# Kernel optimization log

Measured on AMD Instinct MI355X. Metric: run time of the kernel, lower is better.

Reference implementation:

```python
import jax, jax.numpy as jnp
import numpy as np

D_MODEL = 1024
D_STATE = 16
D_CONV = 4
EXPAND = 2
D_INNER = EXPAND * D_MODEL          # 2048
DT_RANK = D_INNER // 16             # 128
BATCH = 2
SEQLEN = 1024


def _silu(x):
    return x * jax.nn.sigmoid(x)


def setup_inputs() -> dict:
    key = jax.random.key(0)
    ks = jax.random.split(key, 8)
    s = 0.02
    A_init = jnp.tile(jnp.arange(1, D_STATE + 1, dtype=jnp.float32)[None, :], (D_INNER, 1))
    return {
        "x": jax.random.normal(ks[0], (BATCH, SEQLEN, D_MODEL), jnp.float32),
        "W_in": jax.random.normal(ks[1], (D_MODEL, 2 * D_INNER), jnp.float32) * s,
        "conv_k": jax.random.normal(ks[2], (D_CONV, 1, D_INNER), jnp.float32) * s,  # (kw, in/groups, out)
        "conv_b": jnp.zeros((D_INNER,), jnp.float32),
        "W_xproj": jax.random.normal(ks[3], (D_INNER, DT_RANK + 2 * D_STATE), jnp.float32) * s,
        "W_dt": jax.random.normal(ks[4], (DT_RANK, D_INNER), jnp.float32) * s,
        "b_dt": jnp.zeros((D_INNER,), jnp.float32),
        "A_log": jnp.log(A_init),
        "D": jnp.ones((D_INNER,), jnp.float32),
        "W_out": jax.random.normal(ks[5], (D_INNER, D_MODEL), jnp.float32) * s,
    }


def reference(x, W_in, conv_k, conv_b, W_xproj, W_dt, b_dt, A_log, D, W_out):
    # in_proj and gate split
    xz = x @ W_in                                   # (B, L, 2*Di)
    x_in, z = jnp.split(xz, 2, axis=-1)             # each (B, L, Di)

    # depthwise causal conv1d: left-pad by d_conv-1 (keras padding='causal')
    xp = jnp.pad(x_in, ((0, 0), (D_CONV - 1, 0), (0, 0)))
    x_in = jax.lax.conv_general_dilated(
        xp, conv_k, window_strides=(1,), padding='VALID',
        dimension_numbers=('NWC', 'WIO', 'NWC'),
        feature_group_count=D_INNER) + conv_b
    u = _silu(x_in)                                 # (B, L, Di)

    # input-dependent SSM params
    x_dbl = u @ W_xproj                             # (B, L, dt_rank + 2*N)
    dt_low, Bm, Cm = jnp.split(x_dbl, [DT_RANK, DT_RANK + D_STATE], axis=-1)
    dt = jax.nn.softplus(dt_low @ W_dt + b_dt)      # (B, L, Di)
    A = -jnp.exp(A_log)                             # (Di, N)
    dA = jnp.exp(jnp.einsum('bld,dn->bldn', dt, A)) # (B, L, Di, N)
    dB = jnp.einsum('bld,bln->bldn', dt, Bm)        # (B, L, Di, N)

    # selective scan over sequence length
    def step(h, e):
        a_t, b_t, u_t, c_t = e                      # (B,Di,N), (B,Di,N), (B,Di), (B,N)
        h = a_t * h + b_t * u_t[..., None]
        y_t = jnp.einsum('bdn,bn->bd', h, c_t)
        return h, y_t

    h0 = jnp.zeros((x.shape[0], D_INNER, D_STATE), dtype=x.dtype)
    xs = (jnp.swapaxes(dA, 0, 1), jnp.swapaxes(dB, 0, 1),
          jnp.swapaxes(u, 0, 1), jnp.swapaxes(Cm, 0, 1))
    _, yT = jax.lax.scan(step, h0, xs)              # (L, B, Di)
    y = jnp.swapaxes(yT, 0, 1) + u * D              # skip connection

    return (y * _silu(z)) @ W_out                   # (B, L, d_model)
```

## Files before the change

### kernel.cpp

```cpp
#include <hip/hip_runtime.h>
#include <hip/hip_bf16.h>

#define D_MODEL 1024
#define D_STATE 16
#define D_CONV 4
#define D_INNER 2048
#define DT_RANK 128
#define BATCH 2
#define SEQLEN 1024
#define XCOLS 160
#define NCHUNK 32
#define LCHUNK 32

typedef __hip_bfloat16 bf16;
typedef __attribute__((ext_vector_type(8))) short short8;
typedef __attribute__((ext_vector_type(4))) float f32x4;

__device__ __forceinline__ unsigned short f2bf_bits(float f) {
    bf16 h = __float2bfloat16(f);
    return *(unsigned short*)&h;
}

__device__ __forceinline__ float softplus_f(float x) {
    return fmaxf(x, 0.f) + __logf(1.f + __expf(-fabsf(x)));
}

__device__ __forceinline__ void load16_lds(void* lds, const void* g) {
    __builtin_amdgcn_global_load_lds(
        (const __attribute__((address_space(1))) unsigned int*)g,
        (__attribute__((address_space(3))) unsigned int*)lds, 16, 0, 0);
}

__device__ __forceinline__ void transpose_tile(const float* __restrict__ B,
                                               bf16* __restrict__ Bt,
                                               int K, int N, int nt, int kt,
                                               float (*t)[33], int tid)
{
    const int tx = tid & 31, ty = tid >> 5;
    const int n0 = nt * 32, k0 = kt * 32;
    #pragma unroll
    for (int r = 0; r < 4; ++r) {
        int n = n0 + tx;
        t[ty + r * 8][tx] = (n < N) ? B[(size_t)(k0 + ty + r * 8) * N + n] : 0.f;
    }
    __syncthreads();
    #pragma unroll
    for (int r = 0; r < 4; ++r)
        Bt[(size_t)(n0 + ty + r * 8) * K + k0 + tx] = __float2bfloat16(t[tx][ty + r * 8]);
}

__global__ __launch_bounds__(256)
void prep_kernel(const float* __restrict__ x, bf16* __restrict__ x_bf,
                 const float* __restrict__ W_in, bf16* __restrict__ Win_t,
                 const float* __restrict__ W_xproj, bf16* __restrict__ Wxp_t,
                 const float* __restrict__ W_dt, bf16* __restrict__ Wdt_t,
                 const float* __restrict__ W_out, bf16* __restrict__ Wout_t,
                 const float* __restrict__ A_log, float* __restrict__ Aneg)
{
    __shared__ float t[32][33];
    const int tid = threadIdx.x;
    int blk = blockIdx.x;
    if (blk < 4096) {
        transpose_tile(W_in, Win_t, D_MODEL, 2 * D_INNER, blk & 127, blk >> 7, t, tid);
        return;
    }
    blk -= 4096;
    if (blk < 512) {
        transpose_tile(W_xproj, Wxp_t, D_INNER, XCOLS, blk & 7, blk >> 3, t, tid);
        return;
    }
    blk -= 512;
    if (blk < 256) {
        transpose_tile(W_dt, Wdt_t, DT_RANK, D_INNER, blk & 63, blk >> 6, t, tid);
        return;
    }
    blk -= 256;
    if (blk < 2048) {
        transpose_tile(W_out, Wout_t, D_INNER, D_MODEL, blk & 31, blk >> 5, t, tid);
        return;
    }
    blk -= 2048;
    if (blk < 2048) {
        int i = blk * 256 + tid;
        float4 v = ((const float4*)x)[i];
        ushort4 p;
        p.x = f2bf_bits(v.x); p.y = f2bf_bits(v.y);
        p.z = f2bf_bits(v.z); p.w = f2bf_bits(v.w);
        ((ushort4*)x_bf)[i] = p;
        return;
    }
    blk -= 2048;
    {
        int i = blk * 256 + tid;
        Aneg[i] = -__expf(A_log[i]);
    }
}

template<int BN, int EPI>
__global__ __launch_bounds__(256)
void gemm_mfma(const bf16* __restrict__ A, const bf16* __restrict__ Bt,
               float* __restrict__ C, bf16* __restrict__ Cb,
               const float* __restrict__ bias,
               int M, int N, int K, int ldc, int kchunk)
{
    constexpr int WN = (BN == 128) ? 64 : 32;
    constexpr int NJ = WN / 16;
    __shared__ short As[128 * 32];
    __shared__ short Bs[BN * 32];
    const int tid = threadIdx.x;
    const int lane = tid & 63, wave = tid >> 6;
    const int wm = (wave >> 1) * 64, wn = (wave & 1) * WN;
    const int row0 = blockIdx.y * 128, col0 = blockIdx.x * BN;
    const int r_m = lane & 15, r_q = lane >> 4;
    const int kstart = blockIdx.z * kchunk;
    float* Cz = C + (size_t)blockIdx.z * M * ldc;

    const int srow = tid >> 2, schk = (tid & 3) * 8;
    const bf16* Ag0 = A  + (size_t)(row0 + srow)      * K + kstart + schk;
    const bf16* Ag1 = A  + (size_t)(row0 + srow + 64) * K + kstart + schk;
    const bf16* Bg0 = Bt + (size_t)(col0 + srow)      * K + kstart + schk;
    const bf16* Bg1 = Bt + (size_t)(col0 + srow + 64) * K + kstart + schk;
    short* AsW0 = &As[8 * tid];
    short* AsW1 = &As[8 * tid + 2048];
    short* BsW0 = &Bs[8 * tid];
    short* BsW1 = &Bs[8 * tid + 2048];

    f32x4 acc[4][NJ];
    #pragma unroll
    for (int i = 0; i < 4; ++i)
        #pragma unroll
        for (int j = 0; j < NJ; ++j)
            #pragma unroll
            for (int r = 0; r < 4; ++r) acc[i][j][r] = 0.f;

    for (int k0 = 0; k0 < kchunk; k0 += 32) {
        __syncthreads();
        load16_lds(AsW0, Ag0 + k0);
        load16_lds(AsW1, Ag1 + k0);
        load16_lds(BsW0, Bg0 + k0);
        if (BN == 128) load16_lds(BsW1, Bg1 + k0);
        __syncthreads();
        short8 af[4], bfr[NJ];
        #pragma unroll
        for (int i = 0; i < 4; ++i)
            af[i] = *(const short8*)&As[(wm + i * 16 + r_m) * 32 + r_q * 8];
        #pragma unroll
        for (int j = 0; j < NJ; ++j)
            bfr[j] = *(const short8*)&Bs[(wn + j * 16 + r_m) * 32 + r_q * 8];
        #pragma unroll
        for (int i = 0; i < 4; ++i)
            #pragma unroll
            for (int j = 0; j < NJ; ++j)
                acc[i][j] = __builtin_amdgcn_mfma_f32_16x16x32_bf16(
                    af[i], bfr[j], acc[i][j], 0, 0, 0);
    }

    #pragma unroll
    for (int i = 0; i < 4; ++i) {
        #pragma unroll
        for (int j = 0; j < NJ; ++j) {
            int row = row0 + wm + i * 16 + r_q * 4;
            int col = col0 + wn + j * 16 + r_m;
            if (col < N) {
                if (EPI == 1) {
                    float bv = bias[col];
                    #pragma unroll
                    for (int r = 0; r < 4; ++r)
                        Cb[(size_t)(row + r) * ldc + col] =
                            __float2bfloat16(softplus_f(acc[i][j][r] + bv));
                } else if (EPI == 2) {
                    if (col < D_INNER) {
                        #pragma unroll
                        for (int r = 0; r < 4; ++r)
                            Cz[(size_t)(row + r) * D_INNER + col] = acc[i][j][r];
                    } else {
                        #pragma unroll
                        for (int r = 0; r < 4; ++r)
                            Cb[(size_t)(row + r) * D_INNER + (col - D_INNER)] =
                                __float2bfloat16(acc[i][j][r]);
                    }
                } else {
                    #pragma unroll
                    for (int r = 0; r < 4; ++r)
                        Cz[(size_t)(row + r) * ldc + col] = acc[i][j][r];
                }
            }
        }
    }
}

__global__ __launch_bounds__(256)
void reduce_xdbl(const float* __restrict__ Cpart, float* __restrict__ x_dbl,
                 bf16* __restrict__ dtA_bf)
{
    int i = blockIdx.x * 256 + threadIdx.x;
    if (i >= 2048 * XCOLS) return;
    int r = i / XCOLS, c = i - r * XCOLS;
    float s = 0.f;
    #pragma unroll
    for (int z = 0; z < 8; ++z)
        s += Cpart[(size_t)z * 2048 * 256 + (size_t)r * 256 + c];
    x_dbl[i] = s;
    if (c < DT_RANK) dtA_bf[(size_t)r * DT_RANK + c] = __float2bfloat16(s);
}

__global__ __launch_bounds__(256)
void reduce_out(const float* __restrict__ Cpart, float* __restrict__ out)
{
    int i = blockIdx.x * 256 + threadIdx.x;
    const float4* p0 = (const float4*)Cpart;
    const float4* p1 = p0 + (size_t)2048 * 1024 / 4;
    float4 a = p0[i], b = p1[i];
    float4 r; r.x = a.x + b.x; r.y = a.y + b.y; r.z = a.z + b.z; r.w = a.w + b.w;
    ((float4*)out)[i] = r;
}

__global__ __launch_bounds__(256)
void conv_silu_kernel(const float* __restrict__ xz32,
                      const float* __restrict__ conv_k,
                      const float* __restrict__ conv_b,
                      bf16* __restrict__ u_bf)
{
    int idx4 = blockIdx.x * 256 + threadIdx.x;
    int d4 = idx4 & (D_INNER / 4 - 1);
    int t = (idx4 >> 9) & (SEQLEN - 1);
    int b = idx4 >> 19;
    float4 acc = ((const float4*)conv_b)[d4];
    #pragma unroll
    for (int k = 0; k < D_CONV; ++k) {
        int tt = t + k - (D_CONV - 1);
        if (tt >= 0) {
            float4 xv = ((const float4*)xz32)[(size_t)(b * SEQLEN + tt) * (D_INNER / 4) + d4];
            float4 kv = ((const float4*)conv_k)[k * (D_INNER / 4) + d4];
            acc.x = fmaf(xv.x, kv.x, acc.x);
            acc.y = fmaf(xv.y, kv.y, acc.y);
            acc.z = fmaf(xv.z, kv.z, acc.z);
            acc.w = fmaf(xv.w, kv.w, acc.w);
        }
    }
    ushort4 pk;
    pk.x = f2bf_bits(acc.x / (1.f + __expf(-acc.x)));
    pk.y = f2bf_bits(acc.y / (1.f + __expf(-acc.y)));
    pk.z = f2bf_bits(acc.z / (1.f + __expf(-acc.z)));
    pk.w = f2bf_bits(acc.w / (1.f + __expf(-acc.w)));
    ((ushort4*)u_bf)[idx4] = pk;
}

__global__ __launch_bounds__(256)
void scan_phase1(const bf16* __restrict__ dt_sb,
                 const float* __restrict__ Aneg,
                 const bf16* __restrict__ u_bf,
                 const float* __restrict__ x_dbl,
                 float* __restrict__ Pst, float* __restrict__ Sst)
{
    __shared__ float Bsm[LCHUNK][16];
    const int d = blockIdx.x * 256 + threadIdx.x;
    const int c = blockIdx.y, b = blockIdx.z;
    const int t0 = c * LCHUNK;
    for (int i = threadIdx.x; i < LCHUNK * 16; i += 256) {
        int tt = i >> 4, n = i & 15;
        Bsm[tt][n] = x_dbl[(size_t)(b * SEQLEN + t0 + tt) * XCOLS + DT_RANK + n];
    }
    float A_row[D_STATE];
    const float4* a4 = (const float4*)(Aneg + d * D_STATE);
    #pragma unroll
    for (int q = 0; q < 4; ++q) {
        float4 v = a4[q];
        A_row[q*4+0] = v.x; A_row[q*4+1] = v.y; A_row[q*4+2] = v.z; A_row[q*4+3] = v.w;
    }
    __syncthreads();
    float P[D_STATE], S[D_STATE];
    #pragma unroll
    for (int n = 0; n < D_STATE; ++n) { P[n] = 1.f; S[n] = 0.f; }
    const bf16* dpp = dt_sb + (size_t)(b * SEQLEN + t0) * D_INNER + d;
    const bf16* upp = u_bf + (size_t)(b * SEQLEN + t0) * D_INNER + d;
    #pragma unroll 8
    for (int t = 0; t < LCHUNK; ++t) {
        float dtv = __bfloat162float(dpp[(size_t)t * D_INNER]);
        float du = dtv * __bfloat162float(upp[(size_t)t * D_INNER]);
        const float4* b4 = (const float4*)&Bsm[t][0];
        #pragma unroll
        for (int q = 0; q < 4; ++q) {
            float4 v = b4[q];
            float Bn[4] = {v.x, v.y, v.z, v.w};
            #pragma unroll
            for (int e = 0; e < 4; ++e) {
                int n = q * 4 + e;
                float a = __expf(dtv * A_row[n]);
                P[n] *= a;
                S[n] = fmaf(a, S[n], du * Bn[e]);
            }
        }
    }
    const size_t base = ((size_t)(b * NCHUNK + c) * D_STATE) * D_INNER + d;
    #pragma unroll
    for (int n = 0; n < D_STATE; ++n) {
        Pst[base + (size_t)n * D_INNER] = P[n];
        Sst[base + (size_t)n * D_INNER] = S[n];
    }
}

__global__ __launch_bounds__(256)
void scan_phase2(const float* __restrict__ Pst, float* __restrict__ Sst)
{
    const int d = blockIdx.x * 256 + threadIdx.x;
    const int n = blockIdx.y;
    const int b = blockIdx.z;
    float h = 0.f;
    for (int c = 0; c < NCHUNK; ++c) {
        const size_t idx = ((size_t)(b * NCHUNK + c) * D_STATE + n) * D_INNER + d;
        float Pv = Pst[idx], Sv = Sst[idx];
        Sst[idx] = h;
        h = fmaf(Pv, h, Sv);
    }
}

__global__ __launch_bounds__(256)
void scan_phase3(const bf16* __restrict__ dt_sb,
                 const float* __restrict__ Aneg,
                 const bf16* __restrict__ u_bf,
                 const float* __restrict__ x_dbl,
                 const float* __restrict__ Dvec,
                 const bf16* __restrict__ z_bf,
                 const float* __restrict__ hin,
                 bf16* __restrict__ g_bf)
{
    __shared__ float BCs[LCHUNK][32];
    const int d = blockIdx.x * 256 + threadIdx.x;
    const int c = blockIdx.y, b = blockIdx.z;
    const int t0 = c * LCHUNK;
    for (int i = threadIdx.x; i < LCHUNK * 32; i += 256) {
        int tt = i >> 5, col = i & 31;
        BCs[tt][col] = x_dbl[(size_t)(b * SEQLEN + t0 + tt) * XCOLS + DT_RANK + col];
    }
    float A_row[D_STATE];
    const float4* a4 = (const float4*)(Aneg + d * D_STATE);
    #pragma unroll
    for (int q = 0; q < 4; ++q) {
        float4 v = a4[q];
        A_row[q*4+0] = v.x; A_row[q*4+1] = v.y; A_row[q*4+2] = v.z; A_row[q*4+3] = v.w;
    }
    const float Dd = Dvec[d];
    __syncthreads();
    float h[D_STATE];
    const size_t base = ((size_t)(b * NCHUNK + c) * D_STATE) * D_INNER + d;
    #pragma unroll
    for (int n = 0; n < D_STATE; ++n) h[n] = hin[base + (size_t)n * D_INNER];
    const bf16* dpp = dt_sb + (size_t)(b * SEQLEN + t0) * D_INNER + d;
    const bf16* upp = u_bf + (size_t)(b * SEQLEN + t0) * D_INNER + d;
    const bf16* zpp = z_bf + (size_t)(b * SEQLEN + t0) * D_INNER + d;
    bf16* gpp = g_bf + (size_t)(b * SEQLEN + t0) * D_INNER + d;
    #pragma unroll 8
    for (int t = 0; t < LCHUNK; ++t) {
        float dtv = __bfloat162float(dpp[(size_t)t * D_INNER]);
        float uv = __bfloat162float(upp[(size_t)t * D_INNER]);
        float zv = __bfloat162float(zpp[(size_t)t * D_INNER]);
        float du = dtv * uv;
        float y = 0.f;
        const float4* bc4 = (const float4*)&BCs[t][0];
        #pragma unroll
        for (int q = 0; q < 4; ++q) {
            float4 v = bc4[q];
            float4 w = bc4[q + 4];
            float Bn[4] = {v.x, v.y, v.z, v.w};
            float Cn[4] = {w.x, w.y, w.z, w.w};
            #pragma unroll
            for (int e = 0; e < 4; ++e) {
                int n = q * 4 + e;
                float a = __expf(dtv * A_row[n]);
                h[n] = fmaf(a, h[n], du * Bn[e]);
                y = fmaf(h[n], Cn[e], y);
            }
        }
        float gy = y + uv * Dd;
        float sz = zv / (1.f + __expf(-zv));
        gpp[(size_t)t * D_INNER] = __float2bfloat16(gy * sz);
    }
}

extern "C" void kernel_launch(void* const* d_in, const int* in_sizes, int n_in,
                              void* d_out, int out_size, void* d_ws, size_t ws_size,
                              hipStream_t stream)
{
    const float* x      = (const float*)d_in[0];
    const float* W_in   = (const float*)d_in[1];
    const float* conv_k = (const float*)d_in[2];
    const float* conv_b = (const float*)d_in[3];
    const float* W_xproj= (const float*)d_in[4];
    const float* W_dt   = (const float*)d_in[5];
    const float* b_dt   = (const float*)d_in[6];
    const float* A_log  = (const float*)d_in[7];
    const float* Dvec   = (const float*)d_in[8];
    const float* W_out  = (const float*)d_in[9];
    float* out = (float*)d_out;

    const int BL = BATCH * SEQLEN;
    const size_t PS_ELEMS = (size_t)BATCH * NCHUNK * D_STATE * D_INNER;

    float* ws     = (float*)d_ws;
    float* xz32   = ws;
    float* x_dbl  = xz32   + (size_t)BL * D_INNER;
    float* Pst    = x_dbl  + (size_t)BL * XCOLS;
    float* Sst    = Pst    + PS_ELEMS;
    float* extraC = Sst    + PS_ELEMS;
    float* Aneg   = extraC + (size_t)4194304;
    float* Cpart3 = Pst;
    float* Cpart6 = Pst;
    bf16*  x_bf   = (bf16*)extraC;
    bf16* Win_t  = (bf16*)(Aneg + 32768);
    bf16* u_bf   = Win_t + (size_t)4096 * 1024;
    bf16* Wxp_t  = u_bf  + (size_t)BL * D_INNER;
    bf16* dtA_bf = Wxp_t + (size_t)256 * 2048;
    bf16* Wdt_t  = dtA_bf+ (size_t)BL * DT_RANK;
    bf16* g_bf   = Wdt_t + (size_t)2048 * 128;
    bf16* Wout_t = g_bf  + (size_t)BL * D_INNER;
    bf16* dt_sb  = Wout_t+ (size_t)1024 * 2048;
    bf16* z_bf   = dt_sb + (size_t)BL * D_INNER;

    prep_kernel<<<4096 + 512 + 256 + 2048 + 2048 + 128, 256, 0, stream>>>(
        x, x_bf, W_in, Win_t, W_xproj, Wxp_t, W_dt, Wdt_t, W_out, Wout_t, A_log, Aneg);

    gemm_mfma<128, 2><<<dim3(32, 16, 1), 256, 0, stream>>>(
        x_bf, Win_t, xz32, z_bf, nullptr, BL, 2 * D_INNER, D_MODEL, D_INNER, D_MODEL);

    conv_silu_kernel<<<(BL * D_INNER / 4) / 256, 256, 0, stream>>>(xz32, conv_k, conv_b, u_bf);

    gemm_mfma<64, 0><<<dim3(4, 16, 8), 256, 0, stream>>>(
        u_bf, Wxp_t, Cpart3, nullptr, nullptr, BL, 256, D_INNER, 256, 256);
    reduce_xdbl<<<(BL * XCOLS + 255) / 256, 256, 0, stream>>>(Cpart3, x_dbl, dtA_bf);

    gemm_mfma<64, 1><<<dim3(32, 16, 1), 256, 0, stream>>>(
        dtA_bf, Wdt_t, nullptr, dt_sb, b_dt, BL, D_INNER, DT_RANK, D_INNER, DT_RANK);

    scan_phase1<<<dim3(D_INNER / 256, NCHUNK, BATCH), 256, 0, stream>>>(
        dt_sb, Aneg, u_bf, x_dbl, Pst, Sst);
    scan_phase2<<<dim3(D_INNER / 256, D_STATE, BATCH), 256, 0, stream>>>(Pst, Sst);
    scan_phase3<<<dim3(D_INNER / 256, NCHUNK, BATCH), 256, 0, stream>>>(
        dt_sb, Aneg, u_bf, x_dbl, Dvec, z_bf, Sst, g_bf);

    gemm_mfma<64, 0><<<dim3(16, 16, 2), 256, 0, stream>>>(
        g_bf, Wout_t, Cpart6, nullptr, nullptr, BL, D_MODEL, D_INNER, D_MODEL, D_MODEL);
    reduce_out<<<(BL * D_MODEL / 4) / 256, 256, 0, stream>>>(Cpart6, out);
}
```

Measured before the change: 255.9 us.

## Split scan state across thread pairs and use shorter, more numerous chunks

The chunked selective scan now uses 64 chunks of 16 steps instead of 32 of 32. Each channel's 16 states are split across two adjacent threads, and phase 3 combines the partial outputs with a shuffle-xor. This quadruples the thread count in phases 1 and 3 to raise occupancy and cut per-thread serial work and register pressure, at the cost of a longer sequential phase 2 and more chunk-state traffic. The workspace layout is also reshuffled so x_bf aliases Sst, since the chunk-state buffers are now larger.

```diff
diff --git a/kernel.cpp b/kernel.cpp
--- a/kernel.cpp
+++ b/kernel.cpp
@@ -9,8 +9,8 @@
 #define BATCH 2
 #define SEQLEN 1024
 #define XCOLS 160
-#define NCHUNK 32
-#define LCHUNK 32
+#define NCHUNK 64
+#define LCHUNK 16
 
 typedef __hip_bfloat16 bf16;
 typedef __attribute__((ext_vector_type(8))) short short8;
@@ -254,49 +254,44 @@
                  float* __restrict__ Pst, float* __restrict__ Sst)
 {
     __shared__ float Bsm[LCHUNK][16];
-    const int d = blockIdx.x * 256 + threadIdx.x;
+    const int half = threadIdx.x & 1;
+    const int d = blockIdx.x * 128 + (threadIdx.x >> 1);
     const int c = blockIdx.y, b = blockIdx.z;
     const int t0 = c * LCHUNK;
-    for (int i = threadIdx.x; i < LCHUNK * 16; i += 256) {
-        int tt = i >> 4, n = i & 15;
+    {
+        int tt = threadIdx.x >> 4, n = threadIdx.x & 15;
         Bsm[tt][n] = x_dbl[(size_t)(b * SEQLEN + t0 + tt) * XCOLS + DT_RANK + n];
     }
-    float A_row[D_STATE];
-    const float4* a4 = (const float4*)(Aneg + d * D_STATE);
-    #pragma unroll
-    for (int q = 0; q < 4; ++q) {
-        float4 v = a4[q];
-        A_row[q*4+0] = v.x; A_row[q*4+1] = v.y; A_row[q*4+2] = v.z; A_row[q*4+3] = v.w;
+    float A_row[8];
+    {
+        const float4* a4 = (const float4*)(Aneg + d * D_STATE + half * 8);
+        float4 v0 = a4[0], v1 = a4[1];
+        A_row[0]=v0.x; A_row[1]=v0.y; A_row[2]=v0.z; A_row[3]=v0.w;
+        A_row[4]=v1.x; A_row[5]=v1.y; A_row[6]=v1.z; A_row[7]=v1.w;
     }
     __syncthreads();
-    float P[D_STATE], S[D_STATE];
-    #pragma unroll
-    for (int n = 0; n < D_STATE; ++n) { P[n] = 1.f; S[n] = 0.f; }
+    float P[8], S[8];
+    #pragma unroll
+    for (int e = 0; e < 8; ++e) { P[e] = 1.f; S[e] = 0.f; }
     const bf16* dpp = dt_sb + (size_t)(b * SEQLEN + t0) * D_INNER + d;
     const bf16* upp = u_bf + (size_t)(b * SEQLEN + t0) * D_INNER + d;
-    #pragma unroll 8
+    #pragma unroll
     for (int t = 0; t < LCHUNK; ++t) {
         float dtv = __bfloat162float(dpp[(size_t)t * D_INNER]);
         float du = dtv * __bfloat162float(upp[(size_t)t * D_INNER]);
-        const float4* b4 = (const float4*)&Bsm[t][0];
-        #pragma unroll
-        for (int q = 0; q < 4; ++q) {
-            float4 v = b4[q];
-            float Bn[4] = {v.x, v.y, v.z, v.w};
-            #pragma unroll
-            for (int e = 0; e < 4; ++e) {
-                int n = q * 4 + e;
-                float a = __expf(dtv * A_row[n]);
-                P[n] *= a;
-                S[n] = fmaf(a, S[n], du * Bn[e]);
-            }
+        const float* brow = &Bsm[t][half * 8];
+        #pragma unroll
+        for (int e = 0; e < 8; ++e) {
+            float a = __expf(dtv * A_row[e]);
+            P[e] *= a;
+            S[e] = fmaf(a, S[e], du * brow[e]);
         }
     }
-    const size_t base = ((size_t)(b * NCHUNK + c) * D_STATE) * D_INNER + d;
-    #pragma unroll
-    for (int n = 0; n < D_STATE; ++n) {
-        Pst[base + (size_t)n * D_INNER] = P[n];
-        Sst[base + (size_t)n * D_INNER] = S[n];
+    const size_t base = ((size_t)(b * NCHUNK + c) * D_STATE + half * 8) * D_INNER + d;
+    #pragma unroll
+    for (int e = 0; e < 8; ++e) {
+        Pst[base + (size_t)e * D_INNER] = P[e];
+        Sst[base + (size_t)e * D_INNER] = S[e];
     }
 }
 
@@ -307,6 +302,7 @@
     const int n = blockIdx.y;
     const int b = blockIdx.z;
     float h = 0.f;
+    #pragma unroll 8
     for (int c = 0; c < NCHUNK; ++c) {
         const size_t idx = ((size_t)(b * NCHUNK + c) * D_STATE + n) * D_INNER + d;
         float Pv = Pst[idx], Sv = Sst[idx];
@@ -326,55 +322,56 @@
                  bf16* __restrict__ g_bf)
 {
     __shared__ float BCs[LCHUNK][32];
-    const int d = blockIdx.x * 256 + threadIdx.x;
+    const int half = threadIdx.x & 1;
+    const int d = blockIdx.x * 128 + (threadIdx.x >> 1);
     const int c = blockIdx.y, b = blockIdx.z;
     const int t0 = c * LCHUNK;
-    for (int i = threadIdx.x; i < LCHUNK * 32; i += 256) {
-        int tt = i >> 5, col = i & 31;
+    {
+        int i0 = threadIdx.x;
+        int tt = i0 >> 5, col = i0 & 31;
         BCs[tt][col] = x_dbl[(size_t)(b * SEQLEN + t0 + tt) * XCOLS + DT_RANK + col];
-    }
-    float A_row[D_STATE];
-    const float4* a4 = (const float4*)(Aneg + d * D_STATE);
-    #pragma unroll
-    for (int q = 0; q < 4; ++q) {
-        float4 v = a4[q];
-        A_row[q*4+0] = v.x; A_row[q*4+1] = v.y; A_row[q*4+2] = v.z; A_row[q*4+3] = v.w;
+        int i1 = i0 + 256;
+        tt = i1 >> 5; col = i1 & 31;
+        BCs[tt][col] = x_dbl[(size_t)(b * SEQLEN + t0 + tt) * XCOLS + DT_RANK + col];
+    }
+    float A_row[8];
+    {
+        const float4* a4 = (const float4*)(Aneg + d * D_STATE + half * 8);
+        float4 v0 = a4[0], v1 = a4[1];
+        A_row[0]=v0.x; A_row[1]=v0.y; A_row[2]=v0.z; A_row[3]=v0.w;
+        A_row[4]=v1.x; A_row[5]=v1.y; A_row[6]=v1.z; A_row[7]=v1.w;
     }
     const float Dd = Dvec[d];
     __syncthreads();
-    float h[D_STATE];
-    const size_t base = ((size_t)(b * NCHUNK + c) * D_STATE) * D_INNER + d;
-    #pragma unroll
-    for (int n = 0; n < D_STATE; ++n) h[n] = hin[base + (size_t)n * D_INNER];
+    float h[8];
+    const size_t base = ((size_t)(b * NCHUNK + c) * D_STATE + half * 8) * D_INNER + d;
+    #pragma unroll
+    for (int e = 0; e < 8; ++e) h[e] = hin[base + (size_t)e * D_INNER];
     const bf16* dpp = dt_sb + (size_t)(b * SEQLEN + t0) * D_INNER + d;
     const bf16* upp = u_bf + (size_t)(b * SEQLEN + t0) * D_INNER + d;
     const bf16* zpp = z_bf + (size_t)(b * SEQLEN + t0) * D_INNER + d;
     bf16* gpp = g_bf + (size_t)(b * SEQLEN + t0) * D_INNER + d;
-    #pragma unroll 8
+    #pragma unroll
     for (int t = 0; t < LCHUNK; ++t) {
         float dtv = __bfloat162float(dpp[(size_t)t * D_INNER]);
         float uv = __bfloat162float(upp[(size_t)t * D_INNER]);
-        float zv = __bfloat162float(zpp[(size_t)t * D_INNER]);
         float du = dtv * uv;
         float y = 0.f;
-        const float4* bc4 = (const float4*)&BCs[t][0];
-        #pragma unroll
-        for (int q = 0; q < 4; ++q) {
-            float4 v = bc4[q];
-            float4 w = bc4[q + 4];
-            float Bn[4] = {v.x, v.y, v.z, v.w};
-            float Cn[4] = {w.x, w.y, w.z, w.w};
-            #pragma unroll
-            for (int e = 0; e < 4; ++e) {
-                int n = q * 4 + e;
-                float a = __expf(dtv * A_row[n]);
-                h[n] = fmaf(a, h[n], du * Bn[e]);
-                y = fmaf(h[n], Cn[e], y);
-            }
+        const float* brow = &BCs[t][half * 8];
+        const float* crow = &BCs[t][16 + half * 8];
+        #pragma unroll
+        for (int e = 0; e < 8; ++e) {
+            float a = __expf(dtv * A_row[e]);
+            h[e] = fmaf(a, h[e], du * brow[e]);
+            y = fmaf(h[e], crow[e], y);
         }
-        float gy = y + uv * Dd;
-        float sz = zv / (1.f + __expf(-zv));
-        gpp[(size_t)t * D_INNER] = __float2bfloat16(gy * sz);
+        y += __shfl_xor(y, 1, 64);
+        if (half == 0) {
+            float zv = __bfloat162float(zpp[(size_t)t * D_INNER]);
+            float gy = y + uv * Dd;
+            float sz = zv / (1.f + __expf(-zv));
+            gpp[(size_t)t * D_INNER] = __float2bfloat16(gy * sz);
+        }
     }
 }
 
@@ -402,11 +399,10 @@
     float* x_dbl  = xz32   + (size_t)BL * D_INNER;
     float* Pst    = x_dbl  + (size_t)BL * XCOLS;
     float* Sst    = Pst    + PS_ELEMS;
-    float* extraC = Sst    + PS_ELEMS;
-    float* Aneg   = extraC + (size_t)4194304;
+    float* Aneg   = Sst    + PS_ELEMS;
     float* Cpart3 = Pst;
     float* Cpart6 = Pst;
-    bf16*  x_bf   = (bf16*)extraC;
+    bf16*  x_bf   = (bf16*)Sst;
     bf16* Win_t  = (bf16*)(Aneg + 32768);
     bf16* u_bf   = Win_t + (size_t)4096 * 1024;
     bf16* Wxp_t  = u_bf  + (size_t)BL * D_INNER;
@@ -432,10 +428,10 @@
     gemm_mfma<64, 1><<<dim3(32, 16, 1), 256, 0, stream>>>(
         dtA_bf, Wdt_t, nullptr, dt_sb, b_dt, BL, D_INNER, DT_RANK, D_INNER, DT_RANK);
 
-    scan_phase1<<<dim3(D_INNER / 256, NCHUNK, BATCH), 256, 0, stream>>>(
+    scan_phase1<<<dim3(D_INNER / 128, NCHUNK, BATCH), 256, 0, stream>>>(
         dt_sb, Aneg, u_bf, x_dbl, Pst, Sst);
     scan_phase2<<<dim3(D_INNER / 256, D_STATE, BATCH), 256, 0, stream>>>(Pst, Sst);
-    scan_phase3<<<dim3(D_INNER / 256, NCHUNK, BATCH), 256, 0, stream>>>(
+    scan_phase3<<<dim3(D_INNER / 128, NCHUNK, BATCH), 256, 0, stream>>>(
         dt_sb, Aneg, u_bf, x_dbl, Dvec, z_bf, Sst, g_bf);
 
     gemm_mfma<64, 0><<<dim3(16, 16, 2), 256, 0, stream>>>(
```

New measurement: 237.1 us. 1.08x faster.

## Fuse three-phase chunked selective scan into one kernel with LDS carry propagation

Applied to the files above, without the earlier changes.

Replaces the three scan kernels (per-chunk summary, cross-chunk carry, per-chunk output) with a single kernel. Each block owns 4 channels across all 64 chunks of 16 steps and exchanges chunk products and sums through shared memory instead of global buffers. dt and u are kept in registers between the two passes, so they are read from global memory only once. In exchange, each wave accesses only 4 contiguous channels, which gives poorly coalesced bf16 loads. B and C are now read straight from global memory per thread, and the serial carry pass uses only 64 threads while the other threads wait at the barrier.

```diff
diff --git a/kernel.cpp b/kernel.cpp
--- a/kernel.cpp
+++ b/kernel.cpp
@@ -9,8 +9,8 @@
 #define BATCH 2
 #define SEQLEN 1024
 #define XCOLS 160
-#define NCHUNK 32
-#define LCHUNK 32
+#define NCHUNK 64
+#define LCHUNK 16
 
 typedef __hip_bfloat16 bf16;
 typedef __attribute__((ext_vector_type(8))) short short8;
@@ -246,39 +246,46 @@
     ((ushort4*)u_bf)[idx4] = pk;
 }
 
-__global__ __launch_bounds__(256)
-void scan_phase1(const bf16* __restrict__ dt_sb,
-                 const float* __restrict__ Aneg,
-                 const bf16* __restrict__ u_bf,
-                 const float* __restrict__ x_dbl,
-                 float* __restrict__ Pst, float* __restrict__ Sst)
-{
-    __shared__ float Bsm[LCHUNK][16];
-    const int d = blockIdx.x * 256 + threadIdx.x;
-    const int c = blockIdx.y, b = blockIdx.z;
+#define PSIDX(c, n, dd) ((c) * 68 + (n) * 4 + (dd))
+__global__ __launch_bounds__(256)
+void scan_fused(const bf16* __restrict__ dt_sb,
+                const float* __restrict__ Aneg,
+                const bf16* __restrict__ u_bf,
+                const float* __restrict__ x_dbl,
+                const float* __restrict__ Dvec,
+                const bf16* __restrict__ z_bf,
+                bf16* __restrict__ g_bf)
+{
+    __shared__ float Pl[64 * 68];
+    __shared__ float Sl[64 * 68];
+    const int tid = threadIdx.x;
+    const int dd = tid & 3, c = tid >> 2;
+    const int d = blockIdx.x * 4 + dd;
+    const int b = blockIdx.z;
     const int t0 = c * LCHUNK;
-    for (int i = threadIdx.x; i < LCHUNK * 16; i += 256) {
-        int tt = i >> 4, n = i & 15;
-        Bsm[tt][n] = x_dbl[(size_t)(b * SEQLEN + t0 + tt) * XCOLS + DT_RANK + n];
-    }
+
     float A_row[D_STATE];
-    const float4* a4 = (const float4*)(Aneg + d * D_STATE);
-    #pragma unroll
-    for (int q = 0; q < 4; ++q) {
-        float4 v = a4[q];
-        A_row[q*4+0] = v.x; A_row[q*4+1] = v.y; A_row[q*4+2] = v.z; A_row[q*4+3] = v.w;
-    }
-    __syncthreads();
-    float P[D_STATE], S[D_STATE];
-    #pragma unroll
-    for (int n = 0; n < D_STATE; ++n) { P[n] = 1.f; S[n] = 0.f; }
+    {
+        const float4* a4 = (const float4*)(Aneg + d * D_STATE);
+        #pragma unroll
+        for (int q = 0; q < 4; ++q) {
+            float4 v = a4[q];
+            A_row[q*4+0]=v.x; A_row[q*4+1]=v.y; A_row[q*4+2]=v.z; A_row[q*4+3]=v.w;
+        }
+    }
+
     const bf16* dpp = dt_sb + (size_t)(b * SEQLEN + t0) * D_INNER + d;
     const bf16* upp = u_bf + (size_t)(b * SEQLEN + t0) * D_INNER + d;
-    #pragma unroll 8
+    float dtv[LCHUNK], uv[LCHUNK];
+    float P[D_STATE], S[D_STATE];
+    #pragma unroll
+    for (int n = 0; n < D_STATE; ++n) { P[n] = 1.f; S[n] = 0.f; }
+    #pragma unroll
     for (int t = 0; t < LCHUNK; ++t) {
-        float dtv = __bfloat162float(dpp[(size_t)t * D_INNER]);
-        float du = dtv * __bfloat162float(upp[(size_t)t * D_INNER]);
-        const float4* b4 = (const float4*)&Bsm[t][0];
+        dtv[t] = __bfloat162float(dpp[(size_t)t * D_INNER]);
+        uv[t] = __bfloat162float(upp[(size_t)t * D_INNER]);
+        float du = dtv[t] * uv[t];
+        const float4* b4 = (const float4*)(x_dbl + (size_t)(b * SEQLEN + t0 + t) * XCOLS + DT_RANK);
         #pragma unroll
         for (int q = 0; q < 4; ++q) {
             float4 v = b4[q];
@@ -286,93 +293,59 @@
             #pragma unroll
             for (int e = 0; e < 4; ++e) {
                 int n = q * 4 + e;
-                float a = __expf(dtv * A_row[n]);
+                float a = __expf(dtv[t] * A_row[n]);
                 P[n] *= a;
                 S[n] = fmaf(a, S[n], du * Bn[e]);
             }
         }
     }
-    const size_t base = ((size_t)(b * NCHUNK + c) * D_STATE) * D_INNER + d;
     #pragma unroll
     for (int n = 0; n < D_STATE; ++n) {
-        Pst[base + (size_t)n * D_INNER] = P[n];
-        Sst[base + (size_t)n * D_INNER] = S[n];
-    }
-}
-
-__global__ __launch_bounds__(256)
-void scan_phase2(const float* __restrict__ Pst, float* __restrict__ Sst)
-{
-    const int d = blockIdx.x * 256 + threadIdx.x;
-    const int n = blockIdx.y;
-    const int b = blockIdx.z;
-    float h = 0.f;
-    for (int c = 0; c < NCHUNK; ++c) {
-        const size_t idx = ((size_t)(b * NCHUNK + c) * D_STATE + n) * D_INNER + d;
-        float Pv = Pst[idx], Sv = Sst[idx];
-        Sst[idx] = h;
-        h = fmaf(Pv, h, Sv);
-    }
-}
-
-__global__ __launch_bounds__(256)
-void scan_phase3(const bf16* __restrict__ dt_sb,
-                 const float* __restrict__ Aneg,
-                 const bf16* __restrict__ u_bf,
-                 const float* __restrict__ x_dbl,
-                 const float* __restrict__ Dvec,
-                 const bf16* __restrict__ z_bf,
-                 const float* __restrict__ hin,
-                 bf16* __restrict__ g_bf)
-{
-    __shared__ float BCs[LCHUNK][32];
-    const int d = blockIdx.x * 256 + threadIdx.x;
-    const int c = blockIdx.y, b = blockIdx.z;
-    const int t0 = c * LCHUNK;
-    for (int i = threadIdx.x; i < LCHUNK * 32; i += 256) {
-        int tt = i >> 5, col = i & 31;
-        BCs[tt][col] = x_dbl[(size_t)(b * SEQLEN + t0 + tt) * XCOLS + DT_RANK + col];
-    }
-    float A_row[D_STATE];
-    const float4* a4 = (const float4*)(Aneg + d * D_STATE);
-    #pragma unroll
-    for (int q = 0; q < 4; ++q) {
-        float4 v = a4[q];
-        A_row[q*4+0] = v.x; A_row[q*4+1] = v.y; A_row[q*4+2] = v.z; A_row[q*4+3] = v.w;
-    }
+        Pl[PSIDX(c, n, dd)] = P[n];
+        Sl[PSIDX(c, n, dd)] = S[n];
+    }
+    __syncthreads();
+
+    if (tid < 64) {
+        const int n2 = tid >> 2, dd2 = tid & 3;
+        float h = 0.f;
+        #pragma unroll 8
+        for (int c2 = 0; c2 < NCHUNK; ++c2) {
+            const int idx = PSIDX(c2, n2, dd2);
+            float Pv = Pl[idx], Sv = Sl[idx];
+            Sl[idx] = h;
+            h = fmaf(Pv, h, Sv);
+        }
+    }
+    __syncthreads();
+
+    float h[D_STATE];
+    #pragma unroll
+    for (int n = 0; n < D_STATE; ++n) h[n] = Sl[PSIDX(c, n, dd)];
     const float Dd = Dvec[d];
-    __syncthreads();
-    float h[D_STATE];
-    const size_t base = ((size_t)(b * NCHUNK + c) * D_STATE) * D_INNER + d;
-    #pragma unroll
-    for (int n = 0; n < D_STATE; ++n) h[n] = hin[base + (size_t)n * D_INNER];
-    const bf16* dpp = dt_sb + (size_t)(b * SEQLEN + t0) * D_INNER + d;
-    const bf16* upp = u_bf + (size_t)(b * SEQLEN + t0) * D_INNER + d;
     const bf16* zpp = z_bf + (size_t)(b * SEQLEN + t0) * D_INNER + d;
     bf16* gpp = g_bf + (size_t)(b * SEQLEN + t0) * D_INNER + d;
-    #pragma unroll 8
+    #pragma unroll
     for (int t = 0; t < LCHUNK; ++t) {
-        float dtv = __bfloat162float(dpp[(size_t)t * D_INNER]);
-        float uv = __bfloat162float(upp[(size_t)t * D_INNER]);
-        float zv = __bfloat162float(zpp[(size_t)t * D_INNER]);
-        float du = dtv * uv;
+        float du = dtv[t] * uv[t];
         float y = 0.f;
-        const float4* bc4 = (const float4*)&BCs[t][0];
+        const float4* b4 = (const float4*)(x_dbl + (size_t)(b * SEQLEN + t0 + t) * XCOLS + DT_RANK);
         #pragma unroll
         for (int q = 0; q < 4; ++q) {
-            float4 v = bc4[q];
-            float4 w = bc4[q + 4];
+            float4 v = b4[q];
+            float4 w = b4[q + 4];
             float Bn[4] = {v.x, v.y, v.z, v.w};
             float Cn[4] = {w.x, w.y, w.z, w.w};
             #pragma unroll
             for (int e = 0; e < 4; ++e) {
                 int n = q * 4 + e;
-                float a = __expf(dtv * A_row[n]);
+                float a = __expf(dtv[t] * A_row[n]);
                 h[n] = fmaf(a, h[n], du * Bn[e]);
                 y = fmaf(h[n], Cn[e], y);
             }
         }
-        float gy = y + uv * Dd;
+        float zv = __bfloat162float(zpp[(size_t)t * D_INNER]);
+        float gy = y + uv[t] * Dd;
         float sz = zv / (1.f + __expf(-zv));
         gpp[(size_t)t * D_INNER] = __float2bfloat16(gy * sz);
     }
@@ -395,18 +368,16 @@
     float* out = (float*)d_out;
 
     const int BL = BATCH * SEQLEN;
-    const size_t PS_ELEMS = (size_t)BATCH * NCHUNK * D_STATE * D_INNER;
 
     float* ws     = (float*)d_ws;
     float* xz32   = ws;
     float* x_dbl  = xz32   + (size_t)BL * D_INNER;
-    float* Pst    = x_dbl  + (size_t)BL * XCOLS;
-    float* Sst    = Pst    + PS_ELEMS;
-    float* extraC = Sst    + PS_ELEMS;
-    float* Aneg   = extraC + (size_t)4194304;
-    float* Cpart3 = Pst;
-    float* Cpart6 = Pst;
-    bf16*  x_bf   = (bf16*)extraC;
+    float* Cbuf   = x_dbl  + (size_t)BL * XCOLS;
+    float* scratch= Cbuf   + (size_t)4194304;
+    float* Aneg   = scratch+ (size_t)4194304;
+    float* Cpart3 = Cbuf;
+    float* Cpart6 = Cbuf;
+    bf16*  x_bf   = (bf16*)scratch;
     bf16* Win_t  = (bf16*)(Aneg + 32768);
     bf16* u_bf   = Win_t + (size_t)4096 * 1024;
     bf16* Wxp_t  = u_bf  + (size_t)BL * D_INNER;
@@ -432,11 +403,8 @@
     gemm_mfma<64, 1><<<dim3(32, 16, 1), 256, 0, stream>>>(
         dtA_bf, Wdt_t, nullptr, dt_sb, b_dt, BL, D_INNER, DT_RANK, D_INNER, DT_RANK);
 
-    scan_phase1<<<dim3(D_INNER / 256, NCHUNK, BATCH), 256, 0, stream>>>(
-        dt_sb, Aneg, u_bf, x_dbl, Pst, Sst);
-    scan_phase2<<<dim3(D_INNER / 256, D_STATE, BATCH), 256, 0, stream>>>(Pst, Sst);
-    scan_phase3<<<dim3(D_INNER / 256, NCHUNK, BATCH), 256, 0, stream>>>(
-        dt_sb, Aneg, u_bf, x_dbl, Dvec, z_bf, Sst, g_bf);
+    scan_fused<<<dim3(D_INNER / 4, 1, BATCH), 256, 0, stream>>>(
+        dt_sb, Aneg, u_bf, x_dbl, Dvec, z_bf, g_bf);
 
     gemm_mfma<64, 0><<<dim3(16, 16, 2), 256, 0, stream>>>(
         g_bf, Wout_t, Cpart6, nullptr, nullptr, BL, D_MODEL, D_INNER, D_MODEL, D_MODEL);
```

New measurement: 291.6 us. +13.9%, slower.

## Halve scan chunk length, pack scan states to bf16, and fuse out-proj reduction via atomics

Applied to the files above, without the earlier changes.

Scan chunks shrink to 16 steps with twice as many chunks, which raises parallelism in phases 1 and 3. The per-chunk P/S states are packed as two bf16 values in one 32-bit word, and the carried-in state is stored as bf16 to cut scan-state traffic. The split-K output GEMM now atomically accumulates into a pre-zeroed output, which removes the separate reduce kernel and the partial buffer. In exchange it adds a memset, makes summation order nondeterministic, and lowers the precision of the chunk-boundary states.

```diff
diff --git a/kernel.cpp b/kernel.cpp
--- a/kernel.cpp
+++ b/kernel.cpp
@@ -9,8 +9,8 @@
 #define BATCH 2
 #define SEQLEN 1024
 #define XCOLS 160
-#define NCHUNK 32
-#define LCHUNK 32
+#define NCHUNK 64
+#define LCHUNK 16
 
 typedef __hip_bfloat16 bf16;
 typedef __attribute__((ext_vector_type(8))) short short8;
@@ -19,6 +19,9 @@
 __device__ __forceinline__ unsigned short f2bf_bits(float f) {
     bf16 h = __float2bfloat16(f);
     return *(unsigned short*)&h;
+}
+__device__ __forceinline__ float bfbits_to_f(unsigned int us) {
+    return __uint_as_float(us << 16);
 }
 
 __device__ __forceinline__ float softplus_f(float x) {
@@ -113,7 +116,7 @@
     const int row0 = blockIdx.y * 128, col0 = blockIdx.x * BN;
     const int r_m = lane & 15, r_q = lane >> 4;
     const int kstart = blockIdx.z * kchunk;
-    float* Cz = C + (size_t)blockIdx.z * M * ldc;
+    float* Cz = (EPI == 3) ? C : C + (size_t)blockIdx.z * M * ldc;
 
     const int srow = tid >> 2, schk = (tid & 3) * 8;
     const bf16* Ag0 = A  + (size_t)(row0 + srow)      * K + kstart + schk;
@@ -179,6 +182,10 @@
                             Cb[(size_t)(row + r) * D_INNER + (col - D_INNER)] =
                                 __float2bfloat16(acc[i][j][r]);
                     }
+                } else if (EPI == 3) {
+                    #pragma unroll
+                    for (int r = 0; r < 4; ++r)
+                        atomicAdd(&Cz[(size_t)(row + r) * ldc + col], acc[i][j][r]);
                 } else {
                     #pragma unroll
                     for (int r = 0; r < 4; ++r)
@@ -202,17 +209,6 @@
         s += Cpart[(size_t)z * 2048 * 256 + (size_t)r * 256 + c];
     x_dbl[i] = s;
     if (c < DT_RANK) dtA_bf[(size_t)r * DT_RANK + c] = __float2bfloat16(s);
-}
-
-__global__ __launch_bounds__(256)
-void reduce_out(const float* __restrict__ Cpart, float* __restrict__ out)
-{
-    int i = blockIdx.x * 256 + threadIdx.x;
-    const float4* p0 = (const float4*)Cpart;
-    const float4* p1 = p0 + (size_t)2048 * 1024 / 4;
-    float4 a = p0[i], b = p1[i];
-    float4 r; r.x = a.x + b.x; r.y = a.y + b.y; r.z = a.z + b.z; r.w = a.w + b.w;
-    ((float4*)out)[i] = r;
 }
 
 __global__ __launch_bounds__(256)
@@ -251,22 +247,24 @@
                  const float* __restrict__ Aneg,
                  const bf16* __restrict__ u_bf,
                  const float* __restrict__ x_dbl,
-                 float* __restrict__ Pst, float* __restrict__ Sst)
+                 unsigned int* __restrict__ PSp)
 {
     __shared__ float Bsm[LCHUNK][16];
     const int d = blockIdx.x * 256 + threadIdx.x;
     const int c = blockIdx.y, b = blockIdx.z;
     const int t0 = c * LCHUNK;
-    for (int i = threadIdx.x; i < LCHUNK * 16; i += 256) {
-        int tt = i >> 4, n = i & 15;
+    {
+        int tt = threadIdx.x >> 4, n = threadIdx.x & 15;
         Bsm[tt][n] = x_dbl[(size_t)(b * SEQLEN + t0 + tt) * XCOLS + DT_RANK + n];
     }
     float A_row[D_STATE];
-    const float4* a4 = (const float4*)(Aneg + d * D_STATE);
-    #pragma unroll
-    for (int q = 0; q < 4; ++q) {
-        float4 v = a4[q];
-        A_row[q*4+0] = v.x; A_row[q*4+1] = v.y; A_row[q*4+2] = v.z; A_row[q*4+3] = v.w;
+    {
+        const float4* a4 = (const float4*)(Aneg + d * D_STATE);
+        #pragma unroll
+        for (int q = 0; q < 4; ++q) {
+            float4 v = a4[q];
+            A_row[q*4+0]=v.x; A_row[q*4+1]=v.y; A_row[q*4+2]=v.z; A_row[q*4+3]=v.w;
+        }
     }
     __syncthreads();
     float P[D_STATE], S[D_STATE];
@@ -274,7 +272,7 @@
     for (int n = 0; n < D_STATE; ++n) { P[n] = 1.f; S[n] = 0.f; }
     const bf16* dpp = dt_sb + (size_t)(b * SEQLEN + t0) * D_INNER + d;
     const bf16* upp = u_bf + (size_t)(b * SEQLEN + t0) * D_INNER + d;
-    #pragma unroll 8
+    #pragma unroll
     for (int t = 0; t < LCHUNK; ++t) {
         float dtv = __bfloat162float(dpp[(size_t)t * D_INNER]);
         float du = dtv * __bfloat162float(upp[(size_t)t * D_INNER]);
@@ -294,23 +292,25 @@
     }
     const size_t base = ((size_t)(b * NCHUNK + c) * D_STATE) * D_INNER + d;
     #pragma unroll
-    for (int n = 0; n < D_STATE; ++n) {
-        Pst[base + (size_t)n * D_INNER] = P[n];
-        Sst[base + (size_t)n * D_INNER] = S[n];
-    }
-}
-
-__global__ __launch_bounds__(256)
-void scan_phase2(const float* __restrict__ Pst, float* __restrict__ Sst)
+    for (int n = 0; n < D_STATE; ++n)
+        PSp[base + (size_t)n * D_INNER] =
+            ((unsigned int)f2bf_bits(S[n]) << 16) | f2bf_bits(P[n]);
+}
+
+__global__ __launch_bounds__(256)
+void scan_phase2(const unsigned int* __restrict__ PSp, bf16* __restrict__ Hin)
 {
     const int d = blockIdx.x * 256 + threadIdx.x;
     const int n = blockIdx.y;
     const int b = blockIdx.z;
     float h = 0.f;
+    #pragma unroll 8
     for (int c = 0; c < NCHUNK; ++c) {
         const size_t idx = ((size_t)(b * NCHUNK + c) * D_STATE + n) * D_INNER + d;
-        float Pv = Pst[idx], Sv = Sst[idx];
-        Sst[idx] = h;
+        unsigned int ps = PSp[idx];
+        float Pv = bfbits_to_f(ps & 0xffffu);
+        float Sv = bfbits_to_f(ps >> 16);
+        Hin[idx] = __float2bfloat16(h);
         h = fmaf(Pv, h, Sv);
     }
 }
@@ -322,39 +322,45 @@
                  const float* __restrict__ x_dbl,
                  const float* __restrict__ Dvec,
                  const bf16* __restrict__ z_bf,
-                 const float* __restrict__ hin,
+                 const bf16* __restrict__ Hin,
                  bf16* __restrict__ g_bf)
 {
     __shared__ float BCs[LCHUNK][32];
     const int d = blockIdx.x * 256 + threadIdx.x;
     const int c = blockIdx.y, b = blockIdx.z;
     const int t0 = c * LCHUNK;
-    for (int i = threadIdx.x; i < LCHUNK * 32; i += 256) {
-        int tt = i >> 5, col = i & 31;
+    {
+        int i0 = threadIdx.x;
+        int tt = i0 >> 5, col = i0 & 31;
         BCs[tt][col] = x_dbl[(size_t)(b * SEQLEN + t0 + tt) * XCOLS + DT_RANK + col];
+        int i1 = i0 + 256;
+        tt = i1 >> 5; col = i1 & 31;
+        BCs[tt][col] = x_dbl[(size_t)(b * SEQLEN + t0 + tt) * XCOLS + DT_RANK + col];
     }
     float A_row[D_STATE];
-    const float4* a4 = (const float4*)(Aneg + d * D_STATE);
-    #pragma unroll
-    for (int q = 0; q < 4; ++q) {
-        float4 v = a4[q];
-        A_row[q*4+0] = v.x; A_row[q*4+1] = v.y; A_row[q*4+2] = v.z; A_row[q*4+3] = v.w;
+    {
+        const float4* a4 = (const float4*)(Aneg + d * D_STATE);
+        #pragma unroll
+        for (int q = 0; q < 4; ++q) {
+            float4 v = a4[q];
+            A_row[q*4+0]=v.x; A_row[q*4+1]=v.y; A_row[q*4+2]=v.z; A_row[q*4+3]=v.w;
+        }
     }
     const float Dd = Dvec[d];
     __syncthreads();
     float h[D_STATE];
     const size_t base = ((size_t)(b * NCHUNK + c) * D_STATE) * D_INNER + d;
     #pragma unroll
-    for (int n = 0; n < D_STATE; ++n) h[n] = hin[base + (size_t)n * D_INNER];
+    for (int n = 0; n < D_STATE; ++n)
+        h[n] = __bfloat162float(Hin[base + (size_t)n * D_INNER]);
     const bf16* dpp = dt_sb + (size_t)(b * SEQLEN + t0) * D_INNER + d;
     const bf16* upp = u_bf + (size_t)(b * SEQLEN + t0) * D_INNER + d;
     const bf16* zpp = z_bf + (size_t)(b * SEQLEN + t0) * D_INNER + d;
     bf16* gpp = g_bf + (size_t)(b * SEQLEN + t0) * D_INNER + d;
-    #pragma unroll 8
+    #pragma unroll
     for (int t = 0; t < LCHUNK; ++t) {
         float dtv = __bfloat162float(dpp[(size_t)t * D_INNER]);
         float uv = __bfloat162float(upp[(size_t)t * D_INNER]);
-        float zv = __bfloat162float(zpp[(size_t)t * D_INNER]);
         float du = dtv * uv;
         float y = 0.f;
         const float4* bc4 = (const float4*)&BCs[t][0];
@@ -372,6 +378,7 @@
                 y = fmaf(h[n], Cn[e], y);
             }
         }
+        float zv = __bfloat162float(zpp[(size_t)t * D_INNER]);
         float gy = y + uv * Dd;
         float sz = zv / (1.f + __expf(-zv));
         gpp[(size_t)t * D_INNER] = __float2bfloat16(gy * sz);
@@ -400,13 +407,11 @@
     float* ws     = (float*)d_ws;
     float* xz32   = ws;
     float* x_dbl  = xz32   + (size_t)BL * D_INNER;
-    float* Pst    = x_dbl  + (size_t)BL * XCOLS;
-    float* Sst    = Pst    + PS_ELEMS;
-    float* extraC = Sst    + PS_ELEMS;
-    float* Aneg   = extraC + (size_t)4194304;
-    float* Cpart3 = Pst;
-    float* Cpart6 = Pst;
-    bf16*  x_bf   = (bf16*)extraC;
+    float* Cpart3 = x_dbl  + (size_t)BL * XCOLS;
+    unsigned int* PSp = (unsigned int*)(Cpart3 + 4194304);
+    bf16* Hin     = (bf16*)(PSp + PS_ELEMS);
+    float* Aneg   = (float*)(Hin + PS_ELEMS);
+    bf16*  x_bf   = (bf16*)Cpart3;
     bf16* Win_t  = (bf16*)(Aneg + 32768);
     bf16* u_bf   = Win_t + (size_t)4096 * 1024;
     bf16* Wxp_t  = u_bf  + (size_t)BL * D_INNER;
@@ -417,6 +422,7 @@
     bf16* dt_sb  = Wout_t+ (size_t)1024 * 2048;
     bf16* z_bf   = dt_sb + (size_t)BL * D_INNER;
 
+    hipMemsetAsync(out, 0, (size_t)out_size * sizeof(float), stream);
     prep_kernel<<<4096 + 512 + 256 + 2048 + 2048 + 128, 256, 0, stream>>>(
         x, x_bf, W_in, Win_t, W_xproj, Wxp_t, W_dt, Wdt_t, W_out, Wout_t, A_log, Aneg);
 
@@ -433,12 +439,11 @@
         dtA_bf, Wdt_t, nullptr, dt_sb, b_dt, BL, D_INNER, DT_RANK, D_INNER, DT_RANK);
 
     scan_phase1<<<dim3(D_INNER / 256, NCHUNK, BATCH), 256, 0, stream>>>(
-        dt_sb, Aneg, u_bf, x_dbl, Pst, Sst);
-    scan_phase2<<<dim3(D_INNER / 256, D_STATE, BATCH), 256, 0, stream>>>(Pst, Sst);
+        dt_sb, Aneg, u_bf, x_dbl, PSp);
+    scan_phase2<<<dim3(D_INNER / 256, D_STATE, BATCH), 256, 0, stream>>>(PSp, Hin);
     scan_phase3<<<dim3(D_INNER / 256, NCHUNK, BATCH), 256, 0, stream>>>(
-        dt_sb, Aneg, u_bf, x_dbl, Dvec, z_bf, Sst, g_bf);
-
-    gemm_mfma<64, 0><<<dim3(16, 16, 2), 256, 0, stream>>>(
-        g_bf, Wout_t, Cpart6, nullptr, nullptr, BL, D_MODEL, D_INNER, D_MODEL, D_MODEL);
-    reduce_out<<<(BL * D_MODEL / 4) / 256, 256, 0, stream>>>(Cpart6, out);
-}
+        dt_sb, Aneg, u_bf, x_dbl, Dvec, z_bf, Hin, g_bf);
+
+    gemm_mfma<64, 3><<<dim3(16, 16, 2), 256, 0, stream>>>(
+        g_bf, Wout_t, out, nullptr, nullptr, BL, D_MODEL, D_INNER, D_MODEL, D_MODEL);
+}
```

Result: faster. 238.2 us (-6.9%).
